# Kernel optimization log

Hardware: AMD Instinct MI355X
Metric: run time of the kernel (lower is better)

## Reference

```python
import jax, jax.numpy as jnp
import numpy as np

B, C, S, Z, D = 32, 64, 128, 64, 256
VI, VO = 30000, 5000
G = D  # gdim == fdim == encdim == embdim


def setup_inputs() -> dict:
    key = jax.random.key(0)
    ks = jax.random.split(key, 9)
    inptensor = jax.random.randint(ks[0], (B, S), 0, VI, dtype=jnp.int32)
    candtensors = jax.random.randint(ks[1], (B, C, Z), 0, VO, dtype=jnp.int32)
    alignments = jnp.zeros((B, C), dtype=jnp.int32)
    align_entropies = jnp.zeros((B, C), dtype=jnp.float32)
    # embedding tables, padding_idx=0 -> zero row 0
    EmbA = (jax.random.normal(ks[2], (VI, D), dtype=jnp.float32) * 0.02).at[0].set(0.0)
    EmbB = (jax.random.normal(ks[3], (VO, D), dtype=jnp.float32) * 0.02).at[0].set(0.0)
    # FlinA == FlinB (sidessame): Linear(encdim -> fdim) + ReLU
    FW = jax.random.normal(ks[4], (D, D), dtype=jnp.float32) / np.sqrt(D)
    Fb = jnp.zeros((D,), dtype=jnp.float32)
    # Glin1 == Glin2: Linear(2*encdim -> gdim) + ReLU
    GW = jax.random.normal(ks[5], (2 * D, G), dtype=jnp.float32) / np.sqrt(2 * D)
    Gb = jnp.zeros((G,), dtype=jnp.float32)
    # Hlin: Linear(2*gdim -> 1)
    HW = jax.random.normal(ks[6], (2 * G, 1), dtype=jnp.float32) / np.sqrt(2 * G)
    Hb = jnp.zeros((1,), dtype=jnp.float32)
    return {
        'inptensor': inptensor, 'candtensors': candtensors,
        'alignments': alignments, 'align_entropies': align_entropies,
        'EmbA': EmbA, 'EmbB': EmbB, 'FW': FW, 'Fb': Fb,
        'GW': GW, 'Gb': Gb, 'HW': HW, 'Hb': Hb,
    }


def reference(inptensor, candtensors, alignments, align_entropies,
              EmbA, EmbB, FW, Fb, GW, Gb, HW, Hb):
    # dropout p=0.0 -> identity; alignments / align_entropies are unused (as in torch forward)
    a = EmbA[inptensor]          # (b, s, d)
    bb = EmbB[candtensors]       # (b, c, z, d)
    a_m = jax.nn.relu(a @ FW + Fb)    # (b, s, f)
    b_m = jax.nn.relu(bb @ FW + Fb)   # (b, c, z, f)
    e_ij = jnp.einsum('bsd,bczd->bcsz', a_m, b_m)
    alpha_w = jax.nn.softmax(e_ij, axis=2)  # over s
    beta_w = jax.nn.softmax(e_ij, axis=3)   # over z
    # broadcast-multiply-sum expressed as contractions (same math, no 5D tensor)
    alpha_j = jnp.einsum('bcsz,bsd->bczd', alpha_w, a)   # (b, c, z, d)
    beta_i = jnp.einsum('bcsz,bczd->bcsd', beta_w, bb)   # (b, c, s, d)
    a_rep = jnp.broadcast_to(a[:, None, :, :], (a.shape[0], bb.shape[1], a.shape[1], a.shape[2]))
    v_1i = jax.nn.relu(jnp.concatenate([a_rep, beta_i], -1) @ GW + Gb)   # (b, c, s, g)
    v_2j = jax.nn.relu(jnp.concatenate([bb, alpha_j], -1) @ GW + Gb)     # (b, c, z, g)
    v_1 = v_1i.sum(2)   # (b, c, g)
    v_2 = v_2j.sum(2)   # (b, c, g)
    y = (jnp.concatenate([v_1, v_2], -1) @ HW + Hb)[:, :, 0]  # (b, c)
    return y
```

## Files before the change

### kernel.cpp

```cpp
#include <hip/hip_runtime.h>
#include <hip/hip_bf16.h>
#include <math.h>

#define Bc 32
#define Cc 64
#define Sc 128
#define Zc 64
#define Dc 256
#define VOc 5000

typedef __attribute__((ext_vector_type(8))) short v8s;
typedef __attribute__((ext_vector_type(4))) float f4;

union FQ { uint4 q; v8s s; };
struct HL { v8s hi, lo; };

__device__ __forceinline__ unsigned short bf_bits(__hip_bfloat16 h) {
  union { __hip_bfloat16 b; unsigned short u; } cv; cv.b = h; return cv.u;
}

__device__ __forceinline__ void split_hl(float x, unsigned short& h, unsigned short& l) {
  __hip_bfloat16 hh = __float2bfloat16(x);
  float hf = __bfloat162float(hh);
  __hip_bfloat16 ll = __float2bfloat16(x - hf);
  h = bf_bits(hh); l = bf_bits(ll);
}

__device__ __forceinline__ unsigned pack_hl(float x) {
  unsigned short h, l; split_hl(x, h, l);
  return (unsigned)h | ((unsigned)l << 16);
}

__device__ __forceinline__ HL unpack8(uint4 q0, uint4 q1) {
  FQ h, l;
  h.q.x = __builtin_amdgcn_perm(q0.y, q0.x, 0x05040100u);
  h.q.y = __builtin_amdgcn_perm(q0.w, q0.z, 0x05040100u);
  h.q.z = __builtin_amdgcn_perm(q1.y, q1.x, 0x05040100u);
  h.q.w = __builtin_amdgcn_perm(q1.w, q1.z, 0x05040100u);
  l.q.x = __builtin_amdgcn_perm(q0.y, q0.x, 0x07060302u);
  l.q.y = __builtin_amdgcn_perm(q0.w, q0.z, 0x07060302u);
  l.q.z = __builtin_amdgcn_perm(q1.y, q1.x, 0x07060302u);
  l.q.w = __builtin_amdgcn_perm(q1.w, q1.z, 0x07060302u);
  HL r; r.hi = h.s; r.lo = l.s; return r;
}

__device__ __forceinline__ f4 mm3p(v8s ah, v8s al, v8s bh, v8s bl, f4 c) {
  c = __builtin_amdgcn_mfma_f32_16x16x32_bf16(ah, bh, c, 0, 0, 0);
  c = __builtin_amdgcn_mfma_f32_16x16x32_bf16(ah, bl, c, 0, 0, 0);
  c = __builtin_amdgcn_mfma_f32_16x16x32_bf16(al, bh, c, 0, 0, 0);
  return c;
}
__device__ __forceinline__ f4 mm3h(const HL& A, v8s bh, v8s bl, f4 c) {
  return mm3p(A.hi, A.lo, bh, bl, c);
}

__global__ __launch_bounds__(256) void prep_kernel(
    const float* __restrict__ FW, const float* __restrict__ GW,
    unsigned short* __restrict__ WT_hi, unsigned short* __restrict__ WT_lo)
{
  const int j = blockIdx.x, t = threadIdx.x;
  const int seg = j >> 8, n = j & 255;
  float v;
  if (seg == 0) v = FW[(size_t)t * 256 + n];
  else if (seg == 1) v = GW[(size_t)t * 256 + n];
  else v = GW[(size_t)(256 + t) * 256 + n];
  unsigned short h, l; split_hl(v, h, l);
  WT_hi[(size_t)j * 256 + t] = h;
  WT_lo[(size_t)j * 256 + t] = l;
}

__global__ __launch_bounds__(256, 4) void transform_kernel(
    const float* __restrict__ EmbA, const int* __restrict__ inp,
    const float* __restrict__ EmbB,
    const unsigned short* __restrict__ WT_hi, const unsigned short* __restrict__ WT_lo,
    const float* __restrict__ Fb, const float* __restrict__ Gb,
    unsigned short* __restrict__ Am_hi, unsigned short* __restrict__ Am_lo,
    float* __restrict__ Ta,
    unsigned short* __restrict__ UaT_hi, unsigned short* __restrict__ UaT_lo,
    unsigned short* __restrict__ FB_hi, unsigned short* __restrict__ FB_lo,
    float* __restrict__ Tb, unsigned* __restrict__ Ub_hl)
{
  const bool taskA = (blockIdx.x < 64);
  const int rb = taskA ? blockIdx.x : (blockIdx.x - 64);
  const int nrows = taskA ? 4096 : 5000;
  const float* __restrict__ Emb = taskA ? EmbA : EmbB;
  const int* __restrict__ idx = taskA ? inp : nullptr;

  const int cb = blockIdx.y;
  const int row0 = rb * 64;
  const int seg = cb >> 1;
  const int colb = (cb & 1) * 128;

  __shared__ unsigned short As_hi[64 * 40], As_lo[64 * 40];
  __shared__ unsigned short Ws_hi[128 * 40], Ws_lo[128 * 40];

  const int t = threadIdx.x;
  const int w = t >> 6, l = t & 63, a = l & 15, hq = l >> 4;

  f4 acc[8];
#pragma unroll
  for (int nt = 0; nt < 8; ++nt)
#pragma unroll
    for (int r = 0; r < 4; ++r) acc[nt][r] = 0.f;

  for (int k0 = 0; k0 < 256; k0 += 32) {
#pragma unroll
    for (int i = 0; i < 2; ++i) {
      int flat = i * 256 + t;
      int row = flat >> 3, kq = flat & 7;
      int rr = row0 + row; if (rr > nrows - 1) rr = nrows - 1;
      int src = idx ? idx[rr] : rr;
      float4 v = *(const float4*)&Emb[(size_t)src * 256 + k0 + kq * 4];
      unsigned short h0, l0, h1, l1, h2, l2, h3, l3;
      split_hl(v.x, h0, l0); split_hl(v.y, h1, l1);
      split_hl(v.z, h2, l2); split_hl(v.w, h3, l3);
      unsigned short hs[4] = {h0, h1, h2, h3}, ls[4] = {l0, l1, l2, l3};
      *(uint2*)&As_hi[row * 40 + kq * 4] = *(uint2*)hs;
      *(uint2*)&As_lo[row * 40 + kq * 4] = *(uint2*)ls;
    }
#pragma unroll
    for (int i = 0; i < 4; ++i) {
      int flat = i * 256 + t;
      int pl = flat >> 9, rem = flat & 511;
      int n = rem >> 2, q = rem & 3;
      const unsigned short* Wp = pl ? WT_lo : WT_hi;
      uint4 v = *(const uint4*)&Wp[(size_t)(seg * 256 + colb + n) * 256 + k0 + q * 8];
      *(uint4*)&(pl ? Ws_lo : Ws_hi)[n * 40 + q * 8] = v;
    }
    __syncthreads();
    v8s ah = *(const v8s*)&As_hi[(w * 16 + a) * 40 + hq * 8];
    v8s al = *(const v8s*)&As_lo[(w * 16 + a) * 40 + hq * 8];
    __builtin_amdgcn_s_setprio(1);
#pragma unroll
    for (int nt = 0; nt < 8; ++nt) {
      v8s bh = *(const v8s*)&Ws_hi[(nt * 16 + a) * 40 + hq * 8];
      v8s bl = *(const v8s*)&Ws_lo[(nt * 16 + a) * 40 + hq * 8];
      acc[nt] = mm3p(ah, al, bh, bl, acc[nt]);
    }
    __builtin_amdgcn_s_setprio(0);
    __syncthreads();
  }

#pragma unroll
  for (int nt = 0; nt < 8; ++nt) {
    int col = colb + nt * 16 + a;
    float b0 = (seg == 0) ? Fb[col] : ((seg == 1) ? Gb[col] : 0.f);
#pragma unroll
    for (int r = 0; r < 4; ++r) {
      int row = row0 + w * 16 + hq * 4 + r;
      if (row >= nrows) continue;
      float v = acc[nt][r];
      if (seg == 0) {
        unsigned short h, lo2;
        split_hl(fmaxf(v + b0, 0.f), h, lo2);
        (taskA ? Am_hi : FB_hi)[(size_t)row * 256 + col] = h;
        (taskA ? Am_lo : FB_lo)[(size_t)row * 256 + col] = lo2;
      } else if (seg == 1) {
        (taskA ? Ta : Tb)[(size_t)row * 256 + col] = v + b0;
      } else if (!taskA) {
        Ub_hl[(size_t)row * 256 + col] = pack_hl(v);
      } else {
        unsigned short h, lo2;
        split_hl(v, h, lo2);
        size_t o = ((size_t)((row >> 7) * 256 + col)) * 128 + (row & 127);
        UaT_hi[o] = h; UaT_lo[o] = lo2;
      }
    }
  }
}

#define SMEM_WORDS (8704 + 9216 + 1024 + 512 + 128 + 64 + 64 + 8)
#define SMEM_BYTES (SMEM_WORDS * 4)

__global__ __launch_bounds__(512, 4) void fused_kernel(
    const int* __restrict__ cand,
    const unsigned short* __restrict__ Am_hi, const unsigned short* __restrict__ Am_lo,
    const unsigned short* __restrict__ FB_hi, const unsigned short* __restrict__ FB_lo,
    const unsigned short* __restrict__ UaT_hi, const unsigned short* __restrict__ UaT_lo,
    const unsigned* __restrict__ Ub_hl,
    const float* __restrict__ Ta, const float* __restrict__ Tb,
    float* __restrict__ V1, float* __restrict__ V2)
{
  extern __shared__ char smem[];
  unsigned* E    = (unsigned*)smem;
  unsigned* SH   = E + 8704;
  float* vred = (float*)(SH + 9216);
  float* csp  = vred + 1024;
  float* rrcp = csp + 512;
  float* crcp = rrcp + 128;
  int*   cidx = (int*)(crcp + 64);
  float* gmax = (float*)(cidx + 64);
  unsigned short* SHs = (unsigned short*)SH;

  const int bc = ((blockIdx.x & 7) << 8) | (blockIdx.x >> 3);
  const int b = bc >> 6, t = threadIdx.x;
  const int w = t >> 6, l = t & 63, a = l & 15, hq = l >> 4;

  if (t < 64) cidx[t] = cand[(size_t)bc * 64 + t];
  __syncthreads();

  uint4 Ah4[8], Al4[8];
  {
    const size_t ap = ((size_t)(b * 128 + w * 16 + a)) * 256;
#pragma unroll
    for (int ch = 0; ch < 8; ++ch) {
      Ah4[ch] = *(const uint4*)&Am_hi[ap + ch * 32 + hq * 8];
      Al4[ch] = *(const uint4*)&Am_lo[ap + ch * 32 + hq * 8];
    }
  }
  f4 acc[4];
#pragma unroll
  for (int i = 0; i < 4; ++i)
#pragma unroll
    for (int r = 0; r < 4; ++r) acc[i][r] = 0.f;

  for (int h = 0; h < 2; ++h) {
#pragma unroll
    for (int i = 0; i < 2; ++i) {
      int flat = i * 512 + t;
      int z = flat >> 5, c = flat & 31;
      int row = cidx[h * 32 + z];
      *(uint4*)&SHs[z * 264 + c * 8]        = *(const uint4*)&FB_hi[(size_t)row * 256 + c * 8];
      *(uint4*)&SHs[8448 + z * 264 + c * 8] = *(const uint4*)&FB_lo[(size_t)row * 256 + c * 8];
    }
    __syncthreads();
    __builtin_amdgcn_s_setprio(1);
#pragma unroll
    for (int ch = 0; ch < 8; ++ch) {
      int k0 = ch * 32 + hq * 8;
      FQ ahf, alf; ahf.q = Ah4[ch]; alf.q = Al4[ch];
#pragma unroll
      for (int zt2 = 0; zt2 < 2; ++zt2) {
        const int zr = (zt2 * 16 + a) * 264 + k0;
        acc[h * 2 + zt2] = mm3p(ahf.s, alf.s, *(const v8s*)&SHs[zr],
                                *(const v8s*)&SHs[8448 + zr], acc[h * 2 + zt2]);
      }
    }
    __builtin_amdgcn_s_setprio(0);
    __syncthreads();
  }

  {
    float m = -1e30f;
#pragma unroll
    for (int zt = 0; zt < 4; ++zt)
#pragma unroll
      for (int r = 0; r < 4; ++r) m = fmaxf(m, acc[zt][r]);
#pragma unroll
    for (int d = 1; d < 64; d <<= 1) m = fmaxf(m, __shfl_xor(m, d));
    if (l == 0) gmax[w] = m;
    __syncthreads();
    float M = gmax[0];
#pragma unroll
    for (int q = 1; q < 8; ++q) M = fmaxf(M, gmax[q]);

#pragma unroll
    for (int zt = 0; zt < 4; ++zt)
#pragma unroll
      for (int r = 0; r < 4; ++r) acc[zt][r] = __expf(acc[zt][r] - M);

#pragma unroll
    for (int r = 0; r < 4; ++r) {
      float rs = acc[0][r] + acc[1][r] + acc[2][r] + acc[3][r];
      rs += __shfl_xor(rs, 1); rs += __shfl_xor(rs, 2);
      rs += __shfl_xor(rs, 4); rs += __shfl_xor(rs, 8);
      if (a == 0) rrcp[w * 16 + hq * 4 + r] = 1.f / rs;
    }
#pragma unroll
    for (int zt = 0; zt < 4; ++zt) {
      float c = acc[zt][0] + acc[zt][1] + acc[zt][2] + acc[zt][3];
      c += __shfl_xor(c, 16); c += __shfl_xor(c, 32);
      if (l < 16) csp[w * 64 + zt * 16 + l] = c;
    }
#pragma unroll
    for (int zt = 0; zt < 4; ++zt)
#pragma unroll
      for (int r = 0; r < 4; ++r)
        E[(w * 16 + hq * 4 + r) * 68 + zt * 16 + a] = pack_hl(acc[zt][r]);
    __syncthreads();
    if (t < 64) {
      float s = 0.f;
#pragma unroll
      for (int q = 0; q < 8; ++q) s += csp[q * 64 + t];
      crcp[t] = 1.f / s;
    }
    __syncthreads();
  }

  {
    const int zt = w >> 1, gp = w & 1;
    HL af[4];
#pragma unroll
    for (int ch = 0; ch < 4; ++ch) {
      unsigned q[8];
#pragma unroll
      for (int j = 0; j < 8; ++j)
        q[j] = E[(ch * 32 + hq * 8 + j) * 68 + zt * 16 + a];
      uint4 q0; q0.x = q[0]; q0.y = q[1]; q0.z = q[2]; q0.w = q[3];
      uint4 q1; q1.x = q[4]; q1.y = q[5]; q1.z = q[6]; q1.w = q[7];
      af[ch] = unpack8(q0, q1);
    }
    float crz[4]; const float* tbp[4];
#pragma unroll
    for (int r = 0; r < 4; ++r) {
      int z = zt * 16 + hq * 4 + r;
      crz[r] = crcp[z];
      tbp[r] = Tb + (size_t)cidx[z] * 256;
    }
    for (int Q = 0; Q < 4; ++Q) {
#pragma unroll
      for (int i = 0; i < 4; ++i) {
        int idx4 = i * 512 + t;
        int pl = idx4 >> 10, rem = idx4 & 1023;
        int g = rem >> 4, q = rem & 15;
        const unsigned short* up = pl ? UaT_lo : UaT_hi;
        uint4 v = *(const uint4*)&up[((size_t)(b * 256 + Q * 64 + g)) * 128 + q * 8];
        *(uint4*)&SHs[pl * 8704 + g * 136 + q * 8] = v;
      }
      __syncthreads();
      __builtin_amdgcn_s_setprio(1);
#pragma unroll
      for (int gt2 = 0; gt2 < 2; ++gt2) {
        int gloc = (gp * 2 + gt2) * 16 + a;
        int gg = Q * 64 + gloc;
        f4 c = {0.f, 0.f, 0.f, 0.f};
#pragma unroll
        for (int ch = 0; ch < 4; ++ch) {
          int k0 = ch * 32 + hq * 8;
          c = mm3h(af[ch], *(const v8s*)&SHs[gloc * 136 + k0],
                   *(const v8s*)&SHs[8704 + gloc * 136 + k0], c);
        }
        float sv = 0.f;
#pragma unroll
        for (int r = 0; r < 4; ++r)
          sv += fmaxf(fmaf(c[r], crz[r], tbp[r][gg]), 0.f);
        sv += __shfl_xor(sv, 16); sv += __shfl_xor(sv, 32);
        if (l < 16) vred[zt * 256 + gg] = sv;
      }
      __builtin_amdgcn_s_setprio(0);
      __syncthreads();
    }
    if (t < 256)
      V2[(size_t)bc * 256 + t] = vred[t] + vred[256 + t] + vred[512 + t] + vred[768 + t];
  }

  for (int h = 0; h < 2; ++h) {
#pragma unroll
    for (int i = 0; i < 8; ++i) {
      int flat = i * 512 + t;
      int c2 = flat & 3, g = (flat >> 2) & 127;
      int zp = i * 4 + c2;
      unsigned p0 = Ub_hl[(size_t)cidx[zp * 2]     * 256 + h * 128 + g];
      unsigned p1 = Ub_hl[(size_t)cidx[zp * 2 + 1] * 256 + h * 128 + g];
      SH[g * 36 + zp]        = (p0 & 0xffffu) | (p1 << 16);
      SH[4608 + g * 36 + zp] = (p0 >> 16) | (p1 & 0xffff0000u);
    }
    __syncthreads();

    HL af1[2];
#pragma unroll
    for (int ch = 0; ch < 2; ++ch) {
      const unsigned* p = E + (w * 16 + a) * 68 + ch * 32 + hq * 8;
      af1[ch] = unpack8(*(const uint4*)p, *(const uint4*)(p + 4));
    }
    float rr[4]; const float* tap[4];
#pragma unroll
    for (int r = 0; r < 4; ++r) {
      int s = w * 16 + hq * 4 + r;
      rr[r] = rrcp[s];
      tap[r] = Ta + ((size_t)(b * 128 + s)) * 256 + h * 128;
    }
    __builtin_amdgcn_s_setprio(1);
#pragma unroll
    for (int gt = 0; gt < 8; ++gt) {
      int g = gt * 16 + a;
      f4 c = {0.f, 0.f, 0.f, 0.f};
#pragma unroll
      for (int ch = 0; ch < 2; ++ch) {
        int k0 = ch * 32 + hq * 8;
        c = mm3h(af1[ch], *(const v8s*)&SHs[g * 72 + k0],
                 *(const v8s*)&SHs[9216 + g * 72 + k0], c);
      }
      float sv = 0.f;
#pragma unroll
      for (int r = 0; r < 4; ++r)
        sv += fmaxf(fmaf(c[r], rr[r], tap[r][g]), 0.f);
      sv += __shfl_xor(sv, 16); sv += __shfl_xor(sv, 32);
      if (l < 16) vred[w * 128 + g] = sv;
    }
    __builtin_amdgcn_s_setprio(0);
    __syncthreads();
    if (t < 128) {
      float s = 0.f;
#pragma unroll
      for (int q = 0; q < 8; ++q) s += vred[q * 128 + t];
      V1[(size_t)bc * 256 + h * 128 + t] = s;
    }
  }
}

__global__ __launch_bounds__(256) void final_kernel(
    const float* __restrict__ V1, const float* __restrict__ V2,
    const float* __restrict__ HW, const float* __restrict__ Hb,
    float* __restrict__ y)
{
  const int t = threadIdx.x;
  const int w = t >> 6, l = t & 63;
  const int bc = blockIdx.x * 4 + w;
  float4 v1 = *(const float4*)&V1[(size_t)bc * Dc + l * 4];
  float4 h1 = *(const float4*)&HW[l * 4];
  float4 v2 = *(const float4*)&V2[(size_t)bc * Dc + l * 4];
  float4 h2 = *(const float4*)&HW[Dc + l * 4];
  float sum = v1.x * h1.x + v1.y * h1.y + v1.z * h1.z + v1.w * h1.w
            + v2.x * h2.x + v2.y * h2.y + v2.z * h2.z + v2.w * h2.w;
#pragma unroll
  for (int off = 32; off > 0; off >>= 1) sum += __shfl_down(sum, off);
  if (l == 0) y[bc] = sum + Hb[0];
}

extern "C" void kernel_launch(void* const* d_in, const int* in_sizes, int n_in,
                              void* d_out, int out_size, void* d_ws, size_t ws_size,
                              hipStream_t stream) {
  (void)in_sizes; (void)n_in; (void)out_size; (void)ws_size;
  const int*   inp  = (const int*)d_in[0];
  const int*   cand = (const int*)d_in[1];
  const float* EmbA = (const float*)d_in[4];
  const float* EmbB = (const float*)d_in[5];
  const float* FW   = (const float*)d_in[6];
  const float* Fb   = (const float*)d_in[7];
  const float* GW   = (const float*)d_in[8];
  const float* Gb   = (const float*)d_in[9];
  const float* HW   = (const float*)d_in[10];
  const float* Hb   = (const float*)d_in[11];
  float* y = (float*)d_out;

  const size_t nA = (size_t)Bc * Sc * Dc;
  const size_t nB = (size_t)VOc * Dc;
  const size_t nV = (size_t)Bc * Cc * Dc;
  const size_t nW = (size_t)768 * 256;
  char* ws = (char*)d_ws;
  unsigned short* Am_hi = (unsigned short*)ws;              ws += nA * 2;
  unsigned short* Am_lo = (unsigned short*)ws;              ws += nA * 2;
  unsigned short* FB_hi = (unsigned short*)ws;              ws += nB * 2;
  unsigned short* FB_lo = (unsigned short*)ws;              ws += nB * 2;
  unsigned short* UaT_hi = (unsigned short*)ws;             ws += nA * 2;
  unsigned short* UaT_lo = (unsigned short*)ws;             ws += nA * 2;
  unsigned*       Ub_hl  = (unsigned*)ws;                   ws += nB * 4;
  float*          Ta     = (float*)ws;                      ws += nA * 4;
  float*          Tb     = (float*)ws;                      ws += nB * 4;
  float*          V1     = (float*)ws;                      ws += nV * 4;
  float*          V2     = (float*)ws;                      ws += nV * 4;
  unsigned short* WT_hi  = (unsigned short*)ws;             ws += nW * 2;
  unsigned short* WT_lo  = (unsigned short*)ws;

  hipFuncSetAttribute((const void*)fused_kernel,
                      hipFuncAttributeMaxDynamicSharedMemorySize, SMEM_BYTES);

  prep_kernel<<<768, 256, 0, stream>>>(FW, GW, WT_hi, WT_lo);
  transform_kernel<<<dim3(143, 6), 256, 0, stream>>>(
      EmbA, inp, EmbB, WT_hi, WT_lo, Fb, Gb,
      Am_hi, Am_lo, Ta, UaT_hi, UaT_lo, FB_hi, FB_lo, Tb, Ub_hl);
  fused_kernel<<<Bc * Cc, 512, SMEM_BYTES, stream>>>(
      cand, Am_hi, Am_lo, FB_hi, FB_lo, UaT_hi, UaT_lo, Ub_hl, Ta, Tb, V1, V2);
  final_kernel<<<(Bc * Cc) / 4, 256, 0, stream>>>(V1, V2, HW, Hb, y);
}
```

Measured before the change: 269.0 us.

## Register-prefetch next tiles across GEMM stages and coalesce projection epilogue via LDS

Adds register double-buffering to the projection GEMM and to each stage of the fused kernel: the next chunk is loaded from global memory into registers while the current one is computed, then written to shared memory after a barrier. The projection epilogue now stages results in shared memory and writes them out as wide vectorized stores instead of scattered 2-byte stores. The fused kernel stops holding the Am fragments in registers and reloads them from global memory each chunk, and the E row stride shrinks from 68 to 66, which reduces shared memory use. The goal is to hide global load latency and cut uncoalesced stores, at the cost of extra barriers and higher register pressure from the prefetch buffers.

```diff
diff --git a/kernel.cpp b/kernel.cpp
--- a/kernel.cpp
+++ b/kernel.cpp
@@ -91,43 +91,67 @@
   const int seg = cb >> 1;
   const int colb = (cb & 1) * 128;
 
-  __shared__ unsigned short As_hi[64 * 40], As_lo[64 * 40];
-  __shared__ unsigned short Ws_hi[128 * 40], Ws_lo[128 * 40];
+  __shared__ char smL[30720];
+  unsigned short* As_hi = (unsigned short*)smL;
+  unsigned short* As_lo = As_hi + 2560;
+  unsigned short* Ws_hi = As_lo + 2560;
+  unsigned short* Ws_lo = Ws_hi + 5120;
+  unsigned* EP = (unsigned*)smL;
 
   const int t = threadIdx.x;
   const int w = t >> 6, l = t & 63, a = l & 15, hq = l >> 4;
 
+  const int arow = t >> 3, kq = t & 7;
+  int gr0 = row0 + arow;      if (gr0 > nrows - 1) gr0 = nrows - 1;
+  int gr1 = row0 + arow + 32; if (gr1 > nrows - 1) gr1 = nrows - 1;
+  const int src0 = idx ? idx[gr0] : gr0;
+  const int src1 = idx ? idx[gr1] : gr1;
+  const float* ap0 = Emb + (size_t)src0 * 256 + kq * 4;
+  const float* ap1 = Emb + (size_t)src1 * 256 + kq * 4;
+
+  float4 Ac0, Ac1, An0, An1;
+  uint4 Wc[4], Wn[4];
+
+#define LOADA(ch, x0, x1) { x0 = *(const float4*)(ap0 + (ch) * 32); \
+                            x1 = *(const float4*)(ap1 + (ch) * 32); }
+#define LOADW(ch, WX) _Pragma("unroll") \
+  for (int i = 0; i < 4; ++i) { \
+    int flat = i * 256 + t; \
+    int pl = flat >> 9, rem = flat & 511, n = rem >> 2, q = rem & 3; \
+    const unsigned short* Wp = pl ? WT_lo : WT_hi; \
+    WX[i] = *(const uint4*)&Wp[(size_t)(seg * 256 + colb + n) * 256 + (ch) * 32 + q * 8]; \
+  }
+#define WRITEA(x0, x1) { \
+    unsigned short h0[4], l0[4], h1[4], l1[4]; \
+    split_hl(x0.x, h0[0], l0[0]); split_hl(x0.y, h0[1], l0[1]); \
+    split_hl(x0.z, h0[2], l0[2]); split_hl(x0.w, h0[3], l0[3]); \
+    split_hl(x1.x, h1[0], l1[0]); split_hl(x1.y, h1[1], l1[1]); \
+    split_hl(x1.z, h1[2], l1[2]); split_hl(x1.w, h1[3], l1[3]); \
+    *(uint2*)&As_hi[arow * 40 + kq * 4] = *(uint2*)h0; \
+    *(uint2*)&As_lo[arow * 40 + kq * 4] = *(uint2*)l0; \
+    *(uint2*)&As_hi[(arow + 32) * 40 + kq * 4] = *(uint2*)h1; \
+    *(uint2*)&As_lo[(arow + 32) * 40 + kq * 4] = *(uint2*)l1; }
+#define WRITEW(WX) _Pragma("unroll") \
+  for (int i = 0; i < 4; ++i) { \
+    int flat = i * 256 + t; \
+    int pl = flat >> 9, rem = flat & 511, n = rem >> 2, q = rem & 3; \
+    *(uint4*)&(pl ? Ws_lo : Ws_hi)[n * 40 + q * 8] = WX[i]; \
+  }
+
   f4 acc[8];
 #pragma unroll
   for (int nt = 0; nt < 8; ++nt)
 #pragma unroll
     for (int r = 0; r < 4; ++r) acc[nt][r] = 0.f;
 
-  for (int k0 = 0; k0 < 256; k0 += 32) {
-#pragma unroll
-    for (int i = 0; i < 2; ++i) {
-      int flat = i * 256 + t;
-      int row = flat >> 3, kq = flat & 7;
-      int rr = row0 + row; if (rr > nrows - 1) rr = nrows - 1;
-      int src = idx ? idx[rr] : rr;
-      float4 v = *(const float4*)&Emb[(size_t)src * 256 + k0 + kq * 4];
-      unsigned short h0, l0, h1, l1, h2, l2, h3, l3;
-      split_hl(v.x, h0, l0); split_hl(v.y, h1, l1);
-      split_hl(v.z, h2, l2); split_hl(v.w, h3, l3);
-      unsigned short hs[4] = {h0, h1, h2, h3}, ls[4] = {l0, l1, l2, l3};
-      *(uint2*)&As_hi[row * 40 + kq * 4] = *(uint2*)hs;
-      *(uint2*)&As_lo[row * 40 + kq * 4] = *(uint2*)ls;
-    }
-#pragma unroll
-    for (int i = 0; i < 4; ++i) {
-      int flat = i * 256 + t;
-      int pl = flat >> 9, rem = flat & 511;
-      int n = rem >> 2, q = rem & 3;
-      const unsigned short* Wp = pl ? WT_lo : WT_hi;
-      uint4 v = *(const uint4*)&Wp[(size_t)(seg * 256 + colb + n) * 256 + k0 + q * 8];
-      *(uint4*)&(pl ? Ws_lo : Ws_hi)[n * 40 + q * 8] = v;
-    }
-    __syncthreads();
+  LOADA(0, Ac0, Ac1);
+  LOADW(0, Wc);
+  WRITEA(Ac0, Ac1);
+  WRITEW(Wc);
+  __syncthreads();
+
+  for (int ch = 0; ch < 8; ++ch) {
+    if (ch < 7) { LOADA(ch + 1, An0, An1); LOADW(ch + 1, Wn); }
     v8s ah = *(const v8s*)&As_hi[(w * 16 + a) * 40 + hq * 8];
     v8s al = *(const v8s*)&As_lo[(w * 16 + a) * 40 + hq * 8];
     __builtin_amdgcn_s_setprio(1);
@@ -139,37 +163,97 @@
     }
     __builtin_amdgcn_s_setprio(0);
     __syncthreads();
-  }
-
-#pragma unroll
-  for (int nt = 0; nt < 8; ++nt) {
-    int col = colb + nt * 16 + a;
-    float b0 = (seg == 0) ? Fb[col] : ((seg == 1) ? Gb[col] : 0.f);
-#pragma unroll
-    for (int r = 0; r < 4; ++r) {
-      int row = row0 + w * 16 + hq * 4 + r;
-      if (row >= nrows) continue;
-      float v = acc[nt][r];
-      if (seg == 0) {
-        unsigned short h, lo2;
-        split_hl(fmaxf(v + b0, 0.f), h, lo2);
-        (taskA ? Am_hi : FB_hi)[(size_t)row * 256 + col] = h;
-        (taskA ? Am_lo : FB_lo)[(size_t)row * 256 + col] = lo2;
-      } else if (seg == 1) {
-        (taskA ? Ta : Tb)[(size_t)row * 256 + col] = v + b0;
-      } else if (!taskA) {
-        Ub_hl[(size_t)row * 256 + col] = pack_hl(v);
-      } else {
-        unsigned short h, lo2;
-        split_hl(v, h, lo2);
-        size_t o = ((size_t)((row >> 7) * 256 + col)) * 128 + (row & 127);
-        UaT_hi[o] = h; UaT_lo[o] = lo2;
-      }
-    }
-  }
-}
-
-#define SMEM_WORDS (8704 + 9216 + 1024 + 512 + 128 + 64 + 64 + 8)
+    if (ch < 7) {
+      WRITEA(An0, An1);
+      WRITEW(Wn);
+      __syncthreads();
+    }
+  }
+
+  for (int p = 0; p < 2; ++p) {
+#pragma unroll
+    for (int nt4 = 0; nt4 < 4; ++nt4) {
+      int nt = p * 4 + nt4;
+      int lc = nt4 * 16 + a;
+      int col = colb + p * 64 + lc;
+#pragma unroll
+      for (int r = 0; r < 4; ++r) {
+        int lr = w * 16 + hq * 4 + r;
+        float v = acc[nt][r];
+        unsigned word;
+        if (seg == 0)      word = pack_hl(fmaxf(v + Fb[col], 0.f));
+        else if (seg == 1) word = __float_as_uint(v + Gb[col]);
+        else               word = pack_hl(v);
+        int ad = (seg == 2 && taskA) ? (lc * 66 + lr) : (lr * 66 + lc);
+        EP[ad] = word;
+      }
+    }
+    __syncthreads();
+    if (seg == 1) {
+      int lr = t >> 2, c0 = (t & 3) * 16;
+      int grow = row0 + lr;
+      if (grow < nrows) {
+        float* outp = taskA ? Ta : Tb;
+#pragma unroll
+        for (int j = 0; j < 4; ++j) {
+          float x[4];
+#pragma unroll
+          for (int u = 0; u < 4; ++u) x[u] = __uint_as_float(EP[lr * 66 + c0 + j * 4 + u]);
+          *(float4*)&outp[(size_t)grow * 256 + colb + p * 64 + c0 + j * 4] = *(float4*)x;
+        }
+      }
+    } else if (seg == 0 || !taskA) {
+      int lr = t >> 2, c0 = (t & 3) * 16;
+      int grow = row0 + lr;
+      if (grow < nrows) {
+        if (seg == 0) {
+          unsigned short hs[16], ls[16];
+#pragma unroll
+          for (int j = 0; j < 16; ++j) {
+            unsigned word = EP[lr * 66 + c0 + j];
+            hs[j] = (unsigned short)(word & 0xffffu);
+            ls[j] = (unsigned short)(word >> 16);
+          }
+          unsigned short* Hi = taskA ? Am_hi : FB_hi;
+          unsigned short* Lo = taskA ? Am_lo : FB_lo;
+          size_t o = (size_t)grow * 256 + colb + p * 64 + c0;
+          *(uint4*)&Hi[o] = *(uint4*)&hs[0];
+          *(uint4*)&Hi[o + 8] = *(uint4*)&hs[8];
+          *(uint4*)&Lo[o] = *(uint4*)&ls[0];
+          *(uint4*)&Lo[o + 8] = *(uint4*)&ls[8];
+        } else {
+          size_t o = (size_t)grow * 256 + colb + p * 64 + c0;
+#pragma unroll
+          for (int j = 0; j < 4; ++j) {
+            unsigned x[4];
+#pragma unroll
+            for (int u = 0; u < 4; ++u) x[u] = EP[lr * 66 + c0 + j * 4 + u];
+            *(uint4*)&Ub_hl[o + j * 4] = *(uint4*)x;
+          }
+        }
+      }
+    } else {
+      int lc = t >> 2, q = t & 3;
+      int col = colb + p * 64 + lc;
+      int bI = row0 >> 7, sbase = row0 & 127;
+      unsigned short hs[16], ls[16];
+#pragma unroll
+      for (int j = 0; j < 16; ++j) {
+        unsigned word = EP[lc * 66 + q * 16 + j];
+        hs[j] = (unsigned short)(word & 0xffffu);
+        ls[j] = (unsigned short)(word >> 16);
+      }
+      size_t o = ((size_t)(bI * 256 + col)) * 128 + sbase + q * 16;
+      *(uint4*)&UaT_hi[o] = *(uint4*)&hs[0];
+      *(uint4*)&UaT_hi[o + 8] = *(uint4*)&hs[8];
+      *(uint4*)&UaT_lo[o] = *(uint4*)&ls[0];
+      *(uint4*)&UaT_lo[o + 8] = *(uint4*)&ls[8];
+    }
+    __syncthreads();
+  }
+}
+
+#define SMEM_WORDS (8448 + 9216 + 1024 + 512 + 128 + 64 + 64 + 8)
 #define SMEM_BYTES (SMEM_WORDS * 4)
 
 __global__ __launch_bounds__(512, 4) void fused_kernel(
@@ -183,7 +267,7 @@
 {
   extern __shared__ char smem[];
   unsigned* E    = (unsigned*)smem;
-  unsigned* SH   = E + 8704;
+  unsigned* SH   = E + 8448;
   float* vred = (float*)(SH + 9216);
   float* csp  = vred + 1024;
   float* rrcp = csp + 512;
@@ -199,45 +283,50 @@
   if (t < 64) cidx[t] = cand[(size_t)bc * 64 + t];
   __syncthreads();
 
-  uint4 Ah4[8], Al4[8];
+  uint4 fbh[2], fbl[2];
+#define LDFB(h) _Pragma("unroll") \
+  for (int i = 0; i < 2; ++i) { \
+    int flat = i * 512 + t; int z = flat >> 5, c = flat & 31; \
+    int row = cidx[(h) * 32 + z]; \
+    fbh[i] = *(const uint4*)&FB_hi[(size_t)row * 256 + c * 8]; \
+    fbl[i] = *(const uint4*)&FB_lo[(size_t)row * 256 + c * 8]; \
+  }
+#define WRFB() _Pragma("unroll") \
+  for (int i = 0; i < 2; ++i) { \
+    int flat = i * 512 + t; int z = flat >> 5, c = flat & 31; \
+    *(uint4*)&SHs[z * 264 + c * 8] = fbh[i]; \
+    *(uint4*)&SHs[8448 + z * 264 + c * 8] = fbl[i]; \
+  }
+
+  f4 acc[4];
+#pragma unroll
+  for (int i = 0; i < 4; ++i)
+#pragma unroll
+    for (int r = 0; r < 4; ++r) acc[i][r] = 0.f;
+
+  LDFB(0); WRFB();
+  __syncthreads();
   {
     const size_t ap = ((size_t)(b * 128 + w * 16 + a)) * 256;
-#pragma unroll
-    for (int ch = 0; ch < 8; ++ch) {
-      Ah4[ch] = *(const uint4*)&Am_hi[ap + ch * 32 + hq * 8];
-      Al4[ch] = *(const uint4*)&Am_lo[ap + ch * 32 + hq * 8];
-    }
-  }
-  f4 acc[4];
-#pragma unroll
-  for (int i = 0; i < 4; ++i)
-#pragma unroll
-    for (int r = 0; r < 4; ++r) acc[i][r] = 0.f;
-
-  for (int h = 0; h < 2; ++h) {
-#pragma unroll
-    for (int i = 0; i < 2; ++i) {
-      int flat = i * 512 + t;
-      int z = flat >> 5, c = flat & 31;
-      int row = cidx[h * 32 + z];
-      *(uint4*)&SHs[z * 264 + c * 8]        = *(const uint4*)&FB_hi[(size_t)row * 256 + c * 8];
-      *(uint4*)&SHs[8448 + z * 264 + c * 8] = *(const uint4*)&FB_lo[(size_t)row * 256 + c * 8];
-    }
-    __syncthreads();
-    __builtin_amdgcn_s_setprio(1);
-#pragma unroll
-    for (int ch = 0; ch < 8; ++ch) {
-      int k0 = ch * 32 + hq * 8;
-      FQ ahf, alf; ahf.q = Ah4[ch]; alf.q = Al4[ch];
-#pragma unroll
-      for (int zt2 = 0; zt2 < 2; ++zt2) {
-        const int zr = (zt2 * 16 + a) * 264 + k0;
-        acc[h * 2 + zt2] = mm3p(ahf.s, alf.s, *(const v8s*)&SHs[zr],
-                                *(const v8s*)&SHs[8448 + zr], acc[h * 2 + zt2]);
-      }
-    }
-    __builtin_amdgcn_s_setprio(0);
-    __syncthreads();
+    for (int h = 0; h < 2; ++h) {
+      if (h == 0) LDFB(1);
+      __builtin_amdgcn_s_setprio(1);
+#pragma unroll
+      for (int ch = 0; ch < 8; ++ch) {
+        int k0 = ch * 32 + hq * 8;
+        v8s Ah = *(const v8s*)&Am_hi[ap + k0];
+        v8s Al = *(const v8s*)&Am_lo[ap + k0];
+#pragma unroll
+        for (int zt2 = 0; zt2 < 2; ++zt2) {
+          const int zr = (zt2 * 16 + a) * 264 + k0;
+          acc[h * 2 + zt2] = mm3p(Ah, Al, *(const v8s*)&SHs[zr],
+                                  *(const v8s*)&SHs[8448 + zr], acc[h * 2 + zt2]);
+        }
+      }
+      __builtin_amdgcn_s_setprio(0);
+      __syncthreads();
+      if (h == 0) { WRFB(); __syncthreads(); }
+    }
   }
 
   {
@@ -276,7 +365,7 @@
     for (int zt = 0; zt < 4; ++zt)
 #pragma unroll
       for (int r = 0; r < 4; ++r)
-        E[(w * 16 + hq * 4 + r) * 68 + zt * 16 + a] = pack_hl(acc[zt][r]);
+        E[(w * 16 + hq * 4 + r) * 66 + zt * 16 + a] = pack_hl(acc[zt][r]);
     __syncthreads();
     if (t < 64) {
       float s = 0.f;
@@ -295,7 +384,7 @@
       unsigned q[8];
 #pragma unroll
       for (int j = 0; j < 8; ++j)
-        q[j] = E[(ch * 32 + hq * 8 + j) * 68 + zt * 16 + a];
+        q[j] = E[(ch * 32 + hq * 8 + j) * 66 + zt * 16 + a];
       uint4 q0; q0.x = q[0]; q0.y = q[1]; q0.z = q[2]; q0.w = q[3];
       uint4 q1; q1.x = q[4]; q1.y = q[5]; q1.z = q[6]; q1.w = q[7];
       af[ch] = unpack8(q0, q1);
@@ -307,17 +396,24 @@
       crz[r] = crcp[z];
       tbp[r] = Tb + (size_t)cidx[z] * 256;
     }
+    uint4 uq[4];
+#define LDUA(Q) _Pragma("unroll") \
+    for (int i = 0; i < 4; ++i) { \
+      int idx4 = i * 512 + t; \
+      int pl = idx4 >> 10, rem = idx4 & 1023, g = rem >> 4, q = rem & 15; \
+      const unsigned short* up = pl ? UaT_lo : UaT_hi; \
+      uq[i] = *(const uint4*)&up[((size_t)(b * 256 + (Q) * 64 + g)) * 128 + q * 8]; \
+    }
+#define WRUA() _Pragma("unroll") \
+    for (int i = 0; i < 4; ++i) { \
+      int idx4 = i * 512 + t; \
+      int pl = idx4 >> 10, rem = idx4 & 1023, g = rem >> 4, q = rem & 15; \
+      *(uint4*)&SHs[pl * 8704 + g * 136 + q * 8] = uq[i]; \
+    }
+    LDUA(0); WRUA();
+    __syncthreads();
     for (int Q = 0; Q < 4; ++Q) {
-#pragma unroll
-      for (int i = 0; i < 4; ++i) {
-        int idx4 = i * 512 + t;
-        int pl = idx4 >> 10, rem = idx4 & 1023;
-        int g = rem >> 4, q = rem & 15;
-        const unsigned short* up = pl ? UaT_lo : UaT_hi;
-        uint4 v = *(const uint4*)&up[((size_t)(b * 256 + Q * 64 + g)) * 128 + q * 8];
-        *(uint4*)&SHs[pl * 8704 + g * 136 + q * 8] = v;
-      }
-      __syncthreads();
+      if (Q < 3) LDUA(Q + 1);
       __builtin_amdgcn_s_setprio(1);
 #pragma unroll
       for (int gt2 = 0; gt2 < 2; ++gt2) {
@@ -339,28 +435,37 @@
       }
       __builtin_amdgcn_s_setprio(0);
       __syncthreads();
+      if (Q < 3) { WRUA(); __syncthreads(); }
     }
     if (t < 256)
       V2[(size_t)bc * 256 + t] = vred[t] + vred[256 + t] + vred[512 + t] + vred[768 + t];
   }
 
-  for (int h = 0; h < 2; ++h) {
-#pragma unroll
-    for (int i = 0; i < 8; ++i) {
-      int flat = i * 512 + t;
-      int c2 = flat & 3, g = (flat >> 2) & 127;
-      int zp = i * 4 + c2;
-      unsigned p0 = Ub_hl[(size_t)cidx[zp * 2]     * 256 + h * 128 + g];
-      unsigned p1 = Ub_hl[(size_t)cidx[zp * 2 + 1] * 256 + h * 128 + g];
-      SH[g * 36 + zp]        = (p0 & 0xffffu) | (p1 << 16);
-      SH[4608 + g * 36 + zp] = (p0 >> 16) | (p1 & 0xffff0000u);
-    }
+  {
+    unsigned ub0[8], ub1[8];
+#define LDUB(h) _Pragma("unroll") \
+    for (int i = 0; i < 8; ++i) { \
+      int flat = i * 512 + t; \
+      int c2 = flat & 3, g = (flat >> 2) & 127; \
+      int zp = i * 4 + c2; \
+      ub0[i] = Ub_hl[(size_t)cidx[zp * 2]     * 256 + (h) * 128 + g]; \
+      ub1[i] = Ub_hl[(size_t)cidx[zp * 2 + 1] * 256 + (h) * 128 + g]; \
+    }
+#define WRUB() _Pragma("unroll") \
+    for (int i = 0; i < 8; ++i) { \
+      int flat = i * 512 + t; \
+      int c2 = flat & 3, g = (flat >> 2) & 127; \
+      int zp = i * 4 + c2; \
+      SH[g * 36 + zp]        = (ub0[i] & 0xffffu) | (ub1[i] << 16); \
+      SH[4608 + g * 36 + zp] = (ub0[i] >> 16) | (ub1[i] & 0xffff0000u); \
+    }
+    LDUB(0); WRUB();
     __syncthreads();
 
     HL af1[2];
 #pragma unroll
     for (int ch = 0; ch < 2; ++ch) {
-      const unsigned* p = E + (w * 16 + a) * 68 + ch * 32 + hq * 8;
+      const unsigned* p = E + (w * 16 + a) * 66 + ch * 32 + hq * 8;
       af1[ch] = unpack8(*(const uint4*)p, *(const uint4*)(p + 4));
     }
     float rr[4]; const float* tap[4];
@@ -368,33 +473,37 @@
     for (int r = 0; r < 4; ++r) {
       int s = w * 16 + hq * 4 + r;
       rr[r] = rrcp[s];
-      tap[r] = Ta + ((size_t)(b * 128 + s)) * 256 + h * 128;
-    }
-    __builtin_amdgcn_s_setprio(1);
-#pragma unroll
-    for (int gt = 0; gt < 8; ++gt) {
-      int g = gt * 16 + a;
-      f4 c = {0.f, 0.f, 0.f, 0.f};
-#pragma unroll
-      for (int ch = 0; ch < 2; ++ch) {
-        int k0 = ch * 32 + hq * 8;
-        c = mm3h(af1[ch], *(const v8s*)&SHs[g * 72 + k0],
-                 *(const v8s*)&SHs[9216 + g * 72 + k0], c);
-      }
-      float sv = 0.f;
-#pragma unroll
-      for (int r = 0; r < 4; ++r)
-        sv += fmaxf(fmaf(c[r], rr[r], tap[r][g]), 0.f);
-      sv += __shfl_xor(sv, 16); sv += __shfl_xor(sv, 32);
-      if (l < 16) vred[w * 128 + g] = sv;
-    }
-    __builtin_amdgcn_s_setprio(0);
-    __syncthreads();
-    if (t < 128) {
-      float s = 0.f;
-#pragma unroll
-      for (int q = 0; q < 8; ++q) s += vred[q * 128 + t];
-      V1[(size_t)bc * 256 + h * 128 + t] = s;
+      tap[r] = Ta + ((size_t)(b * 128 + s)) * 256;
+    }
+    for (int h = 0; h < 2; ++h) {
+      if (h == 0) LDUB(1);
+      __builtin_amdgcn_s_setprio(1);
+#pragma unroll
+      for (int gt = 0; gt < 8; ++gt) {
+        int g = gt * 16 + a;
+        f4 c = {0.f, 0.f, 0.f, 0.f};
+#pragma unroll
+        for (int ch = 0; ch < 2; ++ch) {
+          int k0 = ch * 32 + hq * 8;
+          c = mm3h(af1[ch], *(const v8s*)&SHs[g * 72 + k0],
+                   *(const v8s*)&SHs[9216 + g * 72 + k0], c);
+        }
+        float sv = 0.f;
+#pragma unroll
+        for (int r = 0; r < 4; ++r)
+          sv += fmaxf(fmaf(c[r], rr[r], tap[r][h * 128 + g]), 0.f);
+        sv += __shfl_xor(sv, 16); sv += __shfl_xor(sv, 32);
+        if (l < 16) vred[w * 128 + g] = sv;
+      }
+      __builtin_amdgcn_s_setprio(0);
+      __syncthreads();
+      if (t < 128) {
+        float s = 0.f;
+#pragma unroll
+        for (int q = 0; q < 8; ++q) s += vred[q * 128 + t];
+        V1[(size_t)bc * 256 + h * 128 + t] = s;
+      }
+      if (h == 0) { __syncthreads(); WRUB(); __syncthreads(); }
     }
   }
 }
```

After: 351.3 us. 1.31x slower.
